# Kernel tuning notes

Hardware: AMD Instinct MI355X
Metric: run time of the kernel (lower is better)

Reference implementation:

```python
import jax, jax.numpy as jnp
from jax import lax
import numpy as np

N_VOX = 50000
B = 2
D, H, W = 8, 160, 160
CIN = 16
G = 3
K = 27
CHANS = [(16, 16), (16, 32), (32, 64), (64, 64), (64, 128)]
NAMES = ['in', 'e1', 'e2', 'e3', 'out']


def setup_inputs() -> dict:
    key = jax.random.key(0)
    ks = jax.random.split(key, 16)
    rng = np.random.default_rng(0)
    # unique active cells -> deterministic scatter/gather rulebook
    lin = rng.choice(B * D * H * W, size=N_VOX, replace=False)
    bz = lin // (D * H * W)
    rem = lin % (D * H * W)
    zz = rem // (H * W)
    yy = (rem % (H * W)) // W
    xx = rem % W
    coors = jnp.asarray(np.stack([bz, zz, yy, xx], 1).astype(np.int32))
    inp = {
        'voxel_features': jax.random.normal(ks[0], (N_VOX, CIN), jnp.float32),
        'coors': coors,
        'batch_size': B,
    }
    i = 1
    for nm, (ci, co) in zip(NAMES, CHANS):
        k1, k2 = jax.random.split(ks[i]); i += 1
        inp['wb_' + nm] = jax.random.normal(k1, (K, ci, co), jnp.float32) * 0.05
        inp['ws_' + nm] = jax.random.normal(k2, (K, ci, G, co), jnp.float32) * 0.05
        inp['gm_' + nm] = jnp.ones((co,), jnp.float32)
        inp['bt_' + nm] = jnp.zeros((co,), jnp.float32)
    return inp


def _kan_block(feat, nbr, wb, ws, gm, bt, centers, inv_h):
    # submanifold KAN conv: gather -> (silu base + RBF spline basis) GEMM -> accumulate
    n = feat.shape[0]
    fp = jnp.concatenate([feat, jnp.zeros((1, feat.shape[1]), feat.dtype)], 0)  # pad row for out-of-grid

    def body(acc, kin):
        idx, wbk, wsk = kin
        x = fp[idx]                                   # [N, Cin] gathered neighbors
        base = jax.nn.silu(x) @ wbk                   # [N, Cout]
        bas = jnp.exp(-jnp.square((x[:, :, None] - centers) * inv_h))  # [N, Cin, G]
        spl = jnp.einsum('ncg,cgo->no', bas, wsk)     # [N, Cout]
        return acc + base + spl, None

    out0 = jnp.zeros((n, wb.shape[-1]), feat.dtype)
    out, _ = lax.scan(jax.checkpoint(body), out0, (nbr, wb, ws))
    # BatchNorm1d (train-mode batch stats) + ReLU
    mu = out.mean(0)
    var = out.var(0)
    out = (out - mu) * lax.rsqrt(var + 1e-3) * gm + bt
    return jax.nn.relu(out)


def _build_rulebook(coors, batch_size, n):
    grid = jnp.full((batch_size, D + 2, H + 2, W + 2), n, jnp.int32)
    grid = grid.at[coors[:, 0], coors[:, 1] + 1, coors[:, 2] + 1, coors[:, 3] + 1].set(
        jnp.arange(n, dtype=jnp.int32))
    offs = [(dz, dy, dx) for dz in (-1, 0, 1) for dy in (-1, 0, 1) for dx in (-1, 0, 1)]
    return jnp.stack([
        grid[coors[:, 0], coors[:, 1] + 1 + dz, coors[:, 2] + 1 + dy, coors[:, 3] + 1 + dx]
        for dz, dy, dx in offs])  # [27, N]


def reference(voxel_features, coors, batch_size,
              wb_in, ws_in, gm_in, bt_in,
              wb_e1, ws_e1, gm_e1, bt_e1,
              wb_e2, ws_e2, gm_e2, bt_e2,
              wb_e3, ws_e3, gm_e3, bt_e3,
              wb_out, ws_out, gm_out, bt_out):
    n = voxel_features.shape[0]
    nbr = _build_rulebook(coors, batch_size, n)
    centers = jnp.linspace(-1.0, 1.0, G)
    inv_h = (G - 1) / 2.0
    x = _kan_block(voxel_features, nbr, wb_in, ws_in, gm_in, bt_in, centers, inv_h)
    x = _kan_block(x, nbr, wb_e1, ws_e1, gm_e1, bt_e1, centers, inv_h)
    x = _kan_block(x, nbr, wb_e2, ws_e2, gm_e2, bt_e2, centers, inv_h)
    x = _kan_block(x, nbr, wb_e3, ws_e3, gm_e3, bt_e3, centers, inv_h)
    x = _kan_block(x, nbr, wb_out, ws_out, gm_out, bt_out, centers, inv_h)
    co = x.shape[1]
    dense = jnp.zeros((batch_size, D, H, W, co), x.dtype)
    dense = dense.at[coors[:, 0], coors[:, 1], coors[:, 2], coors[:, 3]].set(x)
    dense = dense.transpose(0, 4, 1, 2, 3)            # [B, C, D, H, W]
    return dense.reshape(batch_size, co * D, H, W)    # [B, C*D, H, W]
```

## Files before the change

### kernel.cpp

```cpp
#include <hip/hip_runtime.h>

#define N_VOX 50000
#define BATCH 2
#define DD 8
#define HH 160
#define WW 160
#define PD 10
#define PH 162
#define PW 162
#define KK 27
#define NCELL (BATCH*DD*HH*WW)
#define GRID_ELEMS (BATCH*PD*PH*PW)
#define OUT_ELEMS (BATCH*128*DD*HH*WW)

typedef __attribute__((ext_vector_type(8))) short short8v;
typedef __attribute__((ext_vector_type(4))) float float4v;

__device__ inline unsigned short f2bf(float f) {
    unsigned u = __float_as_uint(f);
    u += 0x7FFFu + ((u >> 16) & 1u);
    return (unsigned short)(u >> 16);
}

__device__ inline void gload_lds16(const void* g, void* l) {
    __builtin_amdgcn_global_load_lds(
        (const __attribute__((address_space(1))) void*)g,
        (__attribute__((address_space(3))) void*)l, 16, 0, 0);
}

__global__ void k_flags(const int* __restrict__ coors, int* __restrict__ flags) {
    int n = blockIdx.x * 256 + threadIdx.x;
    if (n >= N_VOX) return;
    int b = coors[n*4+0], z = coors[n*4+1], y = coors[n*4+2], x = coors[n*4+3];
    flags[((b*DD + z)*HH + y)*WW + x] = 1;
}

__global__ void k_scan1(const int* __restrict__ flags, int* __restrict__ scanout,
                        int* __restrict__ bsums) {
    __shared__ int s[256];
    int t = threadIdx.x, blk = blockIdx.x;
    int4 v = ((const int4*)(flags + blk*1024))[t];
    int tsum = v.x + v.y + v.z + v.w;
    s[t] = tsum; __syncthreads();
    for (int off = 1; off < 256; off <<= 1) {
        int x = (t >= off) ? s[t-off] : 0;
        __syncthreads(); s[t] += x; __syncthreads();
    }
    int excl = s[t] - tsum;
    int4 o; o.x = excl; o.y = excl + v.x; o.z = o.y + v.y; o.w = o.z + v.z;
    ((int4*)(scanout + blk*1024))[t] = o;
    if (t == 255) bsums[blk] = s[255];
}

__global__ void k_scan2(int* __restrict__ bsums) {
    __shared__ int s[512];
    int t = threadIdx.x;
    int orig = (t < 400) ? bsums[t] : 0;
    s[t] = orig; __syncthreads();
    for (int off = 1; off < 512; off <<= 1) {
        int x = (t >= off) ? s[t-off] : 0;
        __syncthreads(); s[t] += x; __syncthreads();
    }
    if (t < 400) bsums[t] = s[t] - orig;
}

__global__ void k_pos(const float* __restrict__ vf, const int* __restrict__ coors,
                      const int* __restrict__ scanout, const int* __restrict__ bsums,
                      int* __restrict__ vox_at, int* __restrict__ gridP,
                      unsigned short* __restrict__ phi) {
    int n = blockIdx.x * 256 + threadIdx.x;
    if (n > N_VOX) return;
    if (n == N_VOX) {
        ushort4 p;
        p.x = f2bf(0.f);
        p.y = f2bf(__expf(-1.f));
        p.z = f2bf(1.f);
        p.w = f2bf(__expf(-1.f));
        #pragma unroll
        for (int c = 0; c < 16; ++c)
            *(ushort4*)&phi[((size_t)N_VOX * 16 + c) * 4] = p;
        return;
    }
    int b = coors[n*4+0], z = coors[n*4+1], y = coors[n*4+2], x = coors[n*4+3];
    int lin = ((b*DD + z)*HH + y)*WW + x;
    int pos = scanout[lin] + bsums[lin >> 10];
    vox_at[pos] = n;
    gridP[((b*PD + z+1)*PH + (y+1))*PW + (x+1)] = pos;
    #pragma unroll
    for (int c = 0; c < 16; ++c) {
        float xv = vf[(size_t)n * 16 + c];
        float sig = 1.f / (1.f + __expf(-xv));
        ushort4 p;
        p.x = f2bf(xv * sig);
        p.y = f2bf(__expf(-(xv + 1.f) * (xv + 1.f)));
        p.z = f2bf(__expf(-xv * xv));
        p.w = f2bf(__expf(-(xv - 1.f) * (xv - 1.f)));
        *(ushort4*)&phi[((size_t)pos * 16 + c) * 4] = p;
    }
}

__global__ void k_nbrP(const int* __restrict__ coors, const int* __restrict__ vox_at,
                       const int* __restrict__ gridP, int* __restrict__ nbrP) {
    int i = blockIdx.x * 256 + threadIdx.x;
    if (i >= N_VOX) return;
    int n = vox_at[i];
    int b = coors[n*4+0], z = coors[n*4+1]+1, y = coors[n*4+2]+1, x = coors[n*4+3]+1;
    int k = 0;
    for (int dz = -1; dz <= 1; ++dz)
        for (int dy = -1; dy <= 1; ++dy)
            for (int dx = -1; dx <= 1; ++dx) {
                int g = gridP[((b*PD + z+dz)*PH + (y+dy))*PW + (x+dx)];
                nbrP[k*N_VOX + i] = (g >= 0) ? g : N_VOX;
                ++k;
            }
}

struct WswzArgs {
    const float* wb[5];
    const float* ws[5];
    unsigned short* dst[5];
};
__global__ void k_wswz_all(WswzArgs a) {
    constexpr int off[6]   = {0, 27648, 82944, 304128, 746496, 1631232};
    constexpr int lgCI4[5] = {6, 6, 7, 8, 8};
    constexpr int lgCO[5]  = {4, 5, 6, 6, 7};
    int e = blockIdx.x * 256 + threadIdx.x;
    if (e >= off[5]) return;
    int L = 0;
    #pragma unroll
    for (int i = 1; i < 5; ++i) L += (e >= off[i]);
    int el = e - off[L];
    int CIN4 = 1 << lgCI4[L], COUT = 1 << lgCO[L], CIN = CIN4 >> 2;
    int j8   = el & 7;
    int rest = el >> 3;
    int o    = rest & (COUT - 1);
    int kb   = rest >> lgCO[L];
    int kabs = kb * 8 + j8;
    int k  = kabs >> lgCI4[L];
    int c4 = kabs & (CIN4 - 1);
    int c = c4 >> 2, jj = c4 & 3;
    float v = (jj == 0) ? a.wb[L][(k * CIN + c) * COUT + o]
                        : a.ws[L][((k * CIN + c) * 3 + (jj - 1)) * COUT + o];
    a.dst[L][el] = f2bf(v);
}

template<int CIN, int COUT, int NSPL>
__global__ __launch_bounds__(64, 2) void k_conv_mfma(
    const unsigned short* __restrict__ phi,
    const int*            __restrict__ nbrP,
    const unsigned short* __restrict__ Wsw,
    float*                __restrict__ pre,
    float*                __restrict__ sums)
{
    constexpr int CIN4   = CIN * 4;
    constexpr int BK     = 64;
    constexpr int SPK    = CIN4 / BK;
    constexpr int NSTAGE = KK * SPK;
    constexpr int COUTH  = COUT / NSPL;
    constexpr int NFW    = COUTH / 16;
    constexpr int WR     = 4;
    constexpr int NMB    = (N_VOX + 63) / 64;
    constexpr int NBLK   = NMB * NSPL;
    constexpr int PERX   = (NBLK + 7) / 8;

    int lb = blockIdx.x;
    int linear = (lb & 7) * PERX + (lb >> 3);
    if (linear >= NBLK) return;
    const int mb = linear / NSPL, h = linear % NSPL;

    const int lane = threadIdx.x & 63;
    const int l15 = lane & 15, q = lane >> 4;
    const int base = mb * 64;
    int vg[WR];
    #pragma unroll
    for (int rs = 0; rs < WR; ++rs) vg[rs] = base + rs * 16 + l15;
    const int ob = h * COUTH;

    const unsigned short* bp = Wsw + (size_t)(q * COUT + ob + l15) * 8;

    int rows[WR], rowsN[WR];
    short8v A0[2][WR], A1[2][WR];
    short8v B0[2][NFW], B1[2][NFW];

    auto loadB = [&](int sp, short8v (&Bb)[2][NFW]) {
        #pragma unroll
        for (int kk = 0; kk < 2; ++kk)
            #pragma unroll
            for (int nf = 0; nf < NFW; ++nf)
                Bb[kk][nf] = *(const short8v*)(bp +
                    ((size_t)(sp * 8 + kk * 4) * COUT + nf * 16) * 8);
    };
    auto loadA = [&](int sp, short8v (&Ab)[2][WR]) {
        if (sp % SPK == 0) {
            #pragma unroll
            for (int rs = 0; rs < WR; ++rs) rows[rs] = rowsN[rs];
        }
        const int c4s = (sp % SPK) * BK;
        #pragma unroll
        for (int rs = 0; rs < WR; ++rs) {
            const unsigned short* p = phi + (size_t)rows[rs] * CIN4 + c4s + q * 8;
            Ab[0][rs] = *(const short8v*)p;
            Ab[1][rs] = *(const short8v*)(p + 32);
        }
        if (sp % SPK == 0) {
            int k2 = sp / SPK + 1;
            if (k2 < KK) {
                #pragma unroll
                for (int rs = 0; rs < WR; ++rs)
                    rowsN[rs] = (vg[rs] < N_VOX) ? nbrP[k2 * N_VOX + vg[rs]] : N_VOX;
            }
        }
    };

    float4v acc[WR][NFW];
    #pragma unroll
    for (int rs = 0; rs < WR; ++rs)
        #pragma unroll
        for (int nf = 0; nf < NFW; ++nf)
            acc[rs][nf] = (float4v){0.f, 0.f, 0.f, 0.f};

    auto domfma = [&](const short8v (&Ab)[2][WR], const short8v (&Bb)[2][NFW]) {
        #pragma unroll
        for (int kk = 0; kk < 2; ++kk)
            #pragma unroll
            for (int nf = 0; nf < NFW; ++nf)
                #pragma unroll
                for (int rs = 0; rs < WR; ++rs)
                    acc[rs][nf] = __builtin_amdgcn_mfma_f32_16x16x32_bf16(
                        Ab[kk][rs], Bb[kk][nf], acc[rs][nf], 0, 0, 0);
    };

    #pragma unroll
    for (int rs = 0; rs < WR; ++rs) {
        rows[rs]  = (vg[rs] < N_VOX) ? nbrP[vg[rs]] : N_VOX;
        rowsN[rs] = (vg[rs] < N_VOX) ? nbrP[N_VOX + vg[rs]] : N_VOX;
    }
    loadB(0, B0);
    #pragma unroll
    for (int rs = 0; rs < WR; ++rs) {
        const unsigned short* p = phi + (size_t)rows[rs] * CIN4 + q * 8;
        A0[0][rs] = *(const short8v*)p;
        A0[1][rs] = *(const short8v*)(p + 32);
    }

    #define SLOT(T, Ac, Bc, An, Bn)                                   \
        if ((T) + 1 < NSTAGE) { loadB((T) + 1, Bn); loadA((T) + 1, An); } \
        __builtin_amdgcn_sched_barrier(0);                            \
        domfma(Ac, Bc);

    int s = 0;
    for (; s + 2 <= NSTAGE; s += 2) {
        SLOT(s + 0, A0, B0, A1, B1)
        SLOT(s + 1, A1, B1, A0, B0)
    }
    if constexpr (NSTAGE % 2 != 0) {
        domfma(A0, B0);
    }
    #undef SLOT

    #pragma unroll
    for (int rs = 0; rs < WR; ++rs)
        #pragma unroll
        for (int nf = 0; nf < NFW; ++nf)
            #pragma unroll
            for (int r = 0; r < 4; ++r) {
                int v = base + rs * 16 + q * 4 + r;
                if (v < N_VOX)
                    pre[(size_t)v * COUT + ob + nf * 16 + l15] = acc[rs][nf][r];
            }

    float* S = sums + (blockIdx.x & 7) * 256;
    #pragma unroll
    for (int nf = 0; nf < NFW; ++nf) {
        float s1 = 0.f, s2 = 0.f;
        #pragma unroll
        for (int rs = 0; rs < WR; ++rs)
            #pragma unroll
            for (int r = 0; r < 4; ++r) {
                int v = base + rs * 16 + q * 4 + r;
                if (v < N_VOX) {
                    float a = acc[rs][nf][r];
                    s1 += a; s2 += a * a;
                }
            }
        s1 += __shfl_xor(s1, 16); s1 += __shfl_xor(s1, 32);
        s2 += __shfl_xor(s2, 16); s2 += __shfl_xor(s2, 32);
        if (q == 0) {
            atomicAdd(&S[ob + nf * 16 + l15], s1);
            atomicAdd(&S[COUT + ob + nf * 16 + l15], s2);
        }
    }
}

template<int CIN, int COUT, int NSPL>
__global__ __launch_bounds__(512, 4) void k_conv_bsh(
    const unsigned short* __restrict__ phi,
    const int*            __restrict__ nbrP,
    const unsigned short* __restrict__ Wsw,
    float*                __restrict__ pre,
    float*                __restrict__ sums)
{
    constexpr int CIN4   = CIN * 4;
    constexpr int BK     = 64;
    constexpr int SPK    = CIN4 / BK;
    constexpr int NSTAGE = KK * SPK;
    constexpr int KB_G   = 8 * SPK;
    constexpr int COUTH  = COUT / NSPL;
    constexpr int NFW    = COUTH / 16;
    constexpr int WR     = 2;
    constexpr int NMB    = (N_VOX + 255) / 256;
    constexpr int NBLK   = NMB * NSPL;
    constexpr int PERX   = (NBLK + 7) / 8;
    constexpr int SI     = KB_G / 8;

    __shared__ short8v ldsB[2][KB_G][64];

    int lb = blockIdx.x;
    int linear = (lb & 7) * PERX + (lb >> 3);
    if (linear >= NBLK) return;
    const int mb = linear / NSPL, h = linear % NSPL;

    const int t = threadIdx.x, lane = t & 63, w = t >> 6;
    const int l15 = lane & 15, q = lane >> 4;
    const int base = mb * 256 + w * 32;
    int vg[WR];
    #pragma unroll
    for (int rs = 0; rs < WR; ++rs) vg[rs] = base + rs * 16 + l15;
    const int ob = h * COUTH;

    int rows[WR], rowsN[WR];
    short8v A0[2][WR], A1[2][WR];

    auto stage = [&](int g) {
        #pragma unroll
        for (int j = 0; j < SI; ++j) {
            const int m = w * SI + j;
            gload_lds16(Wsw + ((size_t)(g * KB_G + m) * COUT + ob + lane) * 8,
                        &ldsB[g & 1][m][0]);
        }
    };
    auto loadA = [&](int sp, short8v (&Ab)[2][WR]) {
        if (sp % SPK == 0) {
            #pragma unroll
            for (int rs = 0; rs < WR; ++rs) rows[rs] = rowsN[rs];
        }
        const int c4s = (sp % SPK) * BK;
        #pragma unroll
        for (int rs = 0; rs < WR; ++rs) {
            const unsigned short* p = phi + (size_t)rows[rs] * CIN4 + c4s + q * 8;
            Ab[0][rs] = *(const short8v*)p;
            Ab[1][rs] = *(const short8v*)(p + 32);
        }
        if (sp % SPK == 0) {
            int k2 = sp / SPK + 1;
            if (k2 < KK) {
                #pragma unroll
                for (int rs = 0; rs < WR; ++rs)
                    rowsN[rs] = (vg[rs] < N_VOX) ? nbrP[k2 * N_VOX + vg[rs]] : N_VOX;
            }
        }
    };

    float4v acc[WR][NFW];
    #pragma unroll
    for (int rs = 0; rs < WR; ++rs)
        #pragma unroll
        for (int nf = 0; nf < NFW; ++nf)
            acc[rs][nf] = (float4v){0.f, 0.f, 0.f, 0.f};

    stage(0);
    __builtin_amdgcn_sched_barrier(0);
    #pragma unroll
    for (int rs = 0; rs < WR; ++rs) {
        rows[rs]  = (vg[rs] < N_VOX) ? nbrP[vg[rs]] : N_VOX;
        rowsN[rs] = (vg[rs] < N_VOX) ? nbrP[N_VOX + vg[rs]] : N_VOX;
    }
    #pragma unroll
    for (int rs = 0; rs < WR; ++rs) {
        const unsigned short* p = phi + (size_t)rows[rs] * CIN4 + q * 8;
        A0[0][rs] = *(const short8v*)p;
        A0[1][rs] = *(const short8v*)(p + 32);
    }

    int sp = 0;
    #define SLOTB(SG, Ac, An)                                                 \
    {                                                                         \
        short8v bf[2][NFW];                                                   \
        _Pragma("unroll") for (int kk = 0; kk < 2; ++kk)                      \
        _Pragma("unroll") for (int nf = 0; nf < NFW; ++nf)                    \
            bf[kk][nf] = ldsB[g & 1][(SG) * 8 + kk * 4 + q][nf * 16 + l15];   \
        if (sp + 1 < NSTAGE) loadA(sp + 1, An);                               \
        __builtin_amdgcn_sched_barrier(0);                                    \
        _Pragma("unroll") for (int kk = 0; kk < 2; ++kk)                      \
        _Pragma("unroll") for (int nf = 0; nf < NFW; ++nf)                    \
        _Pragma("unroll") for (int rs = 0; rs < WR; ++rs)                     \
            acc[rs][nf] = __builtin_amdgcn_mfma_f32_16x16x32_bf16(            \
                Ac[kk][rs], bf[kk][nf], acc[rs][nf], 0, 0, 0);                \
        ++sp;                                                                 \
    }

    for (int g = 0; g < KK; ++g) {
        if (g == 0) {
            asm volatile("s_waitcnt vmcnt(8)" ::: "memory");
        } else if (g == KK - 1) {
            asm volatile("s_waitcnt vmcnt(%0)" :: "i"(4 * SPK) : "memory");
        } else {
            asm volatile("s_waitcnt vmcnt(%0)" :: "i"(4 * SPK + 2) : "memory");
        }
        __builtin_amdgcn_sched_barrier(0);
        __builtin_amdgcn_s_barrier();
        __builtin_amdgcn_sched_barrier(0);
        if (g + 1 < KK) stage(g + 1);
        __builtin_amdgcn_sched_barrier(0);
        SLOTB(0, A0, A1)
        SLOTB(1, A1, A0)
        if constexpr (SPK == 4) {
            SLOTB(2, A0, A1)
            SLOTB(3, A1, A0)
        }
    }
    #undef SLOTB

    #pragma unroll
    for (int rs = 0; rs < WR; ++rs)
        #pragma unroll
        for (int nf = 0; nf < NFW; ++nf)
            #pragma unroll
            for (int r = 0; r < 4; ++r) {
                int v = base + rs * 16 + q * 4 + r;
                if (v < N_VOX)
                    pre[(size_t)v * COUT + ob + nf * 16 + l15] = acc[rs][nf][r];
            }

    float* S = sums + (blockIdx.x & 7) * 256;
    #pragma unroll
    for (int nf = 0; nf < NFW; ++nf) {
        float s1 = 0.f, s2 = 0.f;
        #pragma unroll
        for (int rs = 0; rs < WR; ++rs)
            #pragma unroll
            for (int r = 0; r < 4; ++r) {
                int v = base + rs * 16 + q * 4 + r;
                if (v < N_VOX) {
                    float a = acc[rs][nf][r];
                    s1 += a; s2 += a * a;
                }
            }
        s1 += __shfl_xor(s1, 16); s1 += __shfl_xor(s1, 32);
        s2 += __shfl_xor(s2, 16); s2 += __shfl_xor(s2, 32);
        if (q == 0) {
            atomicAdd(&S[ob + nf * 16 + l15], s1);
            atomicAdd(&S[COUT + ob + nf * 16 + l15], s2);
        }
    }
}

template<int COUT>
__global__ void k_bnapply_phi(const float* __restrict__ pre, const float* __restrict__ sums,
                              const float* __restrict__ gm, const float* __restrict__ bt,
                              unsigned short* __restrict__ phi) {
    __shared__ float sc[COUT], sh[COUT];
    int t = threadIdx.x;
    if (t < COUT) {
        float s1 = 0.f, s2 = 0.f;
        #pragma unroll
        for (int xo = 0; xo < 8; ++xo) {
            s1 += sums[xo * 256 + t];
            s2 += sums[xo * 256 + COUT + t];
        }
        float mu  = s1 * (1.f / N_VOX);
        float var = s2 * (1.f / N_VOX) - mu*mu;
        float s = rsqrtf(var + 1e-3f) * gm[t];
        sc[t] = s;
        sh[t] = bt[t] - mu * s;
    }
    __syncthreads();
    int tot = (N_VOX + 1) * COUT;
    for (int e = blockIdx.x*256 + t; e < tot; e += gridDim.x*256) {
        int i = e / COUT, c = e % COUT;
        float x = 0.f;
        if (i < N_VOX) x = fmaxf(pre[(size_t)i*COUT + c] * sc[c] + sh[c], 0.f);
        float sig = 1.f / (1.f + __expf(-x));
        ushort4 p;
        p.x = f2bf(x * sig);
        p.y = f2bf(__expf(-(x + 1.f) * (x + 1.f)));
        p.z = f2bf(__expf(-x * x));
        p.w = f2bf(__expf(-(x - 1.f) * (x - 1.f)));
        *(ushort4*)&phi[(size_t)e * 4] = p;
    }
}

__global__ void k_bnfin(const float* __restrict__ sums, const float* __restrict__ gm,
                        const float* __restrict__ bt, float* __restrict__ scsh) {
    int t = threadIdx.x;
    float s1 = 0.f, s2 = 0.f;
    #pragma unroll
    for (int xo = 0; xo < 8; ++xo) {
        s1 += sums[xo * 256 + t];
        s2 += sums[xo * 256 + 128 + t];
    }
    float mu  = s1 * (1.f / N_VOX);
    float var = s2 * (1.f / N_VOX) - mu*mu;
    float s = rsqrtf(var + 1e-3f) * gm[t];
    scsh[t]       = s;
    scsh[128 + t] = bt[t] - mu * s;
}

__global__ void k_dense(const float* __restrict__ feat, const int* __restrict__ gridP,
                        const float* __restrict__ scsh, float* __restrict__ out) {
    int e4 = blockIdx.x*256 + threadIdx.x;
    if (e4 >= OUT_ELEMS/4) return;
    int e = e4 * 4;
    int x  = e % WW;
    int y  = (e / WW) % HH;
    int cz = (e / (WW*HH)) % (128*DD);
    int b  = e / (WW*HH*128*DD);
    int c = cz >> 3, z = cz & 7;
    float sc = scsh[c], sh = scsh[128 + c];
    const int* gp = &gridP[((b*PD + z+1)*PH + (y+1))*PW + (x+1)];
    int g0 = gp[0], g1 = gp[1], g2 = gp[2], g3 = gp[3];
    float4 o;
    o.x = (g0 >= 0) ? fmaxf(feat[(size_t)g0*128 + c] * sc + sh, 0.f) : 0.f;
    o.y = (g1 >= 0) ? fmaxf(feat[(size_t)g1*128 + c] * sc + sh, 0.f) : 0.f;
    o.z = (g2 >= 0) ? fmaxf(feat[(size_t)g2*128 + c] * sc + sh, 0.f) : 0.f;
    o.w = (g3 >= 0) ? fmaxf(feat[(size_t)g3*128 + c] * sc + sh, 0.f) : 0.f;
    *(float4*)&out[e] = o;
}

template<int CIN, int COUT, int NSPL>
static void run_block(const float* gm, const float* bt,
                      const int* nbrP, unsigned short* phi, const unsigned short* Wsw,
                      float* sums, float* pre, hipStream_t stream) {
    constexpr int NMB  = (N_VOX + 63) / 64;
    constexpr int NBLK = NMB * NSPL;
    constexpr int GRID = ((NBLK + 7) / 8) * 8;
    k_conv_mfma<CIN, COUT, NSPL><<<GRID, 64, 0, stream>>>(phi, nbrP, Wsw, pre, sums);
    k_bnapply_phi<COUT><<<512, 256, 0, stream>>>(pre, sums, gm, bt, phi);
}

template<int CIN, int COUT, int NSPL>
static void run_block_bsh(const float* gm, const float* bt,
                          const int* nbrP, unsigned short* phi, const unsigned short* Wsw,
                          float* sums, float* pre, bool last, hipStream_t stream) {
    constexpr int NMB  = (N_VOX + 255) / 256;
    constexpr int NBLK = NMB * NSPL;
    constexpr int GRID = ((NBLK + 7) / 8) * 8;
    k_conv_bsh<CIN, COUT, NSPL><<<GRID, 512, 0, stream>>>(phi, nbrP, Wsw, pre, sums);
    if (!last)
        k_bnapply_phi<COUT><<<512, 256, 0, stream>>>(pre, sums, gm, bt, phi);
}

extern "C" void kernel_launch(void* const* d_in, const int* in_sizes, int n_in,
                              void* d_out, int out_size, void* d_ws, size_t ws_size,
                              hipStream_t stream) {
    const float* vf    = (const float*)d_in[0];
    const int*   coors = (const int*)d_in[1];
    const float* wb[5] = {(const float*)d_in[3],  (const float*)d_in[7],
                          (const float*)d_in[11], (const float*)d_in[15],
                          (const float*)d_in[19]};
    const float* wsp[5]= {(const float*)d_in[4],  (const float*)d_in[8],
                          (const float*)d_in[12], (const float*)d_in[16],
                          (const float*)d_in[20]};
    const float* gm[5] = {(const float*)d_in[5],  (const float*)d_in[9],
                          (const float*)d_in[13], (const float*)d_in[17],
                          (const float*)d_in[21]};
    const float* bt[5] = {(const float*)d_in[6],  (const float*)d_in[10],
                          (const float*)d_in[14], (const float*)d_in[18],
                          (const float*)d_in[22]};

    char* p = (char*)d_ws;
    auto alloc = [&](size_t bytes) {
        char* r = p;
        p += (bytes + 255) & ~(size_t)255;
        return r;
    };
    int*            flags   = (int*)           alloc((size_t)NCELL * 4);
    int*            scanout = (int*)           alloc((size_t)NCELL * 4);
    int*            bsums   = (int*)           alloc(512 * 4);
    int*            vox_at  = (int*)           alloc((size_t)N_VOX * 4);
    int*            gridP   = (int*)           alloc((size_t)GRID_ELEMS * 4);
    int*            nbrP    = (int*)           alloc((size_t)KK * N_VOX * 4);
    unsigned short* Wsw0    = (unsigned short*)alloc((size_t)KK * 64  * 16  * 2);
    unsigned short* Wsw1    = (unsigned short*)alloc((size_t)KK * 64  * 32  * 2);
    unsigned short* Wsw2    = (unsigned short*)alloc((size_t)KK * 128 * 64  * 2);
    unsigned short* Wsw3    = (unsigned short*)alloc((size_t)KK * 256 * 64  * 2);
    unsigned short* Wsw4    = (unsigned short*)alloc((size_t)KK * 256 * 128 * 2);
    unsigned short* phi     = (unsigned short*)alloc((size_t)(N_VOX + 1) * 256 * 2);
    float*          sumsAll = (float*)         alloc(5 * 8 * 256 * 4);
    float*          pre     = (float*)         alloc((size_t)N_VOX * 128 * 4);
    float*          scsh    = (float*)         alloc(256 * 4);

    hipMemsetAsync(flags, 0, (size_t)NCELL * 4, stream);
    hipMemsetAsync(gridP, 0xFF, (size_t)GRID_ELEMS * 4, stream);
    hipMemsetAsync(sumsAll, 0, 5 * 8 * 256 * 4, stream);

    WswzArgs wa;
    for (int i = 0; i < 5; ++i) { wa.wb[i] = wb[i]; wa.ws[i] = wsp[i]; }
    wa.dst[0] = Wsw0; wa.dst[1] = Wsw1; wa.dst[2] = Wsw2; wa.dst[3] = Wsw3; wa.dst[4] = Wsw4;
    k_wswz_all<<<(1631232 + 255) / 256, 256, 0, stream>>>(wa);

    k_flags<<<(N_VOX+255)/256, 256, 0, stream>>>(coors, flags);
    k_scan1<<<NCELL/1024, 256, 0, stream>>>(flags, scanout, bsums);
    k_scan2<<<1, 512, 0, stream>>>(bsums);
    k_pos  <<<(N_VOX+1+255)/256, 256, 0, stream>>>(vf, coors, scanout, bsums,
                                                   vox_at, gridP, phi);
    k_nbrP <<<(N_VOX+255)/256, 256, 0, stream>>>(coors, vox_at, gridP, nbrP);

    run_block<16, 16, 1>(gm[0], bt[0], nbrP, phi, Wsw0, sumsAll + 0*2048, pre, stream);
    run_block<16, 32, 1>(gm[1], bt[1], nbrP, phi, Wsw1, sumsAll + 1*2048, pre, stream);
    run_block_bsh<32, 64,  1>(gm[2], bt[2], nbrP, phi, Wsw2, sumsAll + 2*2048, pre, false, stream);
    run_block_bsh<64, 64,  1>(gm[3], bt[3], nbrP, phi, Wsw3, sumsAll + 3*2048, pre, false, stream);
    run_block_bsh<64, 128, 2>(gm[4], bt[4], nbrP, phi, Wsw4, sumsAll + 4*2048, pre, true,  stream);

    k_bnfin<<<1, 128, 0, stream>>>(sumsAll + 4*2048, gm[4], bt[4], scsh);
    k_dense<<<(OUT_ELEMS/4 + 255)/256, 256, 0, stream>>>(pre, gridP, scsh, (float*)d_out);
}
```

Before: 614.7 us.

## Store intermediate pre-activations as bf16 and deepen A-operand prefetch to three buffers

For the intermediate blocks, the conv kernels now write pre-BN outputs as bf16 rather than fp32, and the BN-apply kernel reads them back as bf16. This halves that write and read traffic. The last block still writes fp32 for the dense scatter. The bsh conv kernel also gains a third A register buffer so gathered neighbour rows are prefetched two stages ahead, and each stage's B fragment loads are split into two halves; this costs more registers and adds bf16 rounding of the pre-BN values.

```diff
diff --git a/kernel.cpp b/kernel.cpp
--- a/kernel.cpp
+++ b/kernel.cpp
@@ -20,6 +20,9 @@
     unsigned u = __float_as_uint(f);
     u += 0x7FFFu + ((u >> 16) & 1u);
     return (unsigned short)(u >> 16);
+}
+__device__ inline float bf2f(unsigned short b) {
+    return __uint_as_float((unsigned)b << 16);
 }
 
 __device__ inline void gload_lds16(const void* g, void* l) {
@@ -149,7 +152,7 @@
     const unsigned short* __restrict__ phi,
     const int*            __restrict__ nbrP,
     const unsigned short* __restrict__ Wsw,
-    float*                __restrict__ pre,
+    unsigned short*       __restrict__ preB,
     float*                __restrict__ sums)
 {
     constexpr int CIN4   = CIN * 4;
@@ -266,7 +269,7 @@
             for (int r = 0; r < 4; ++r) {
                 int v = base + rs * 16 + q * 4 + r;
                 if (v < N_VOX)
-                    pre[(size_t)v * COUT + ob + nf * 16 + l15] = acc[rs][nf][r];
+                    preB[(size_t)v * COUT + ob + nf * 16 + l15] = f2bf(acc[rs][nf][r]);
             }
 
     float* S = sums + (blockIdx.x & 7) * 256;
@@ -292,12 +295,13 @@
     }
 }
 
-template<int CIN, int COUT, int NSPL>
+template<int CIN, int COUT, int NSPL, bool LAST>
 __global__ __launch_bounds__(512, 4) void k_conv_bsh(
     const unsigned short* __restrict__ phi,
     const int*            __restrict__ nbrP,
     const unsigned short* __restrict__ Wsw,
-    float*                __restrict__ pre,
+    float*                __restrict__ preF,
+    unsigned short*       __restrict__ preB,
     float*                __restrict__ sums)
 {
     constexpr int CIN4   = CIN * 4;
@@ -329,7 +333,7 @@
     const int ob = h * COUTH;
 
     int rows[WR], rowsN[WR];
-    short8v A0[2][WR], A1[2][WR];
+    short8v A0[2][WR], A1[2][WR], A2[2][WR];
 
     auto stage = [&](int g) {
         #pragma unroll
@@ -381,45 +385,58 @@
         A0[0][rs] = *(const short8v*)p;
         A0[1][rs] = *(const short8v*)(p + 32);
     }
-
-    int sp = 0;
-    #define SLOTB(SG, Ac, An)                                                 \
+    loadA(1, A1);
+
+    int sp = 0, g = 0;
+
+    #define SLOTX(Ac, An)                                                     \
     {                                                                         \
-        short8v bf[2][NFW];                                                   \
-        _Pragma("unroll") for (int kk = 0; kk < 2; ++kk)                      \
+        const int SG = sp % SPK; const int gb = g & 1;                        \
+        short8v bfv[NFW];                                                     \
         _Pragma("unroll") for (int nf = 0; nf < NFW; ++nf)                    \
-            bf[kk][nf] = ldsB[g & 1][(SG) * 8 + kk * 4 + q][nf * 16 + l15];   \
-        if (sp + 1 < NSTAGE) loadA(sp + 1, An);                               \
+            bfv[nf] = ldsB[gb][SG * 8 + q][nf * 16 + l15];                    \
+        if (sp + 2 < NSTAGE) loadA(sp + 2, An);                               \
         __builtin_amdgcn_sched_barrier(0);                                    \
-        _Pragma("unroll") for (int kk = 0; kk < 2; ++kk)                      \
         _Pragma("unroll") for (int nf = 0; nf < NFW; ++nf)                    \
         _Pragma("unroll") for (int rs = 0; rs < WR; ++rs)                     \
             acc[rs][nf] = __builtin_amdgcn_mfma_f32_16x16x32_bf16(            \
-                Ac[kk][rs], bf[kk][nf], acc[rs][nf], 0, 0, 0);                \
+                Ac[0][rs], bfv[nf], acc[rs][nf], 0, 0, 0);                    \
+        _Pragma("unroll") for (int nf = 0; nf < NFW; ++nf)                    \
+            bfv[nf] = ldsB[gb][SG * 8 + 4 + q][nf * 16 + l15];                \
+        _Pragma("unroll") for (int nf = 0; nf < NFW; ++nf)                    \
+        _Pragma("unroll") for (int rs = 0; rs < WR; ++rs)                     \
+            acc[rs][nf] = __builtin_amdgcn_mfma_f32_16x16x32_bf16(            \
+                Ac[1][rs], bfv[nf], acc[rs][nf], 0, 0, 0);                    \
         ++sp;                                                                 \
     }
 
-    for (int g = 0; g < KK; ++g) {
-        if (g == 0) {
-            asm volatile("s_waitcnt vmcnt(8)" ::: "memory");
-        } else if (g == KK - 1) {
-            asm volatile("s_waitcnt vmcnt(%0)" :: "i"(4 * SPK) : "memory");
+    #define GHDR                                                              \
+        if (g == 0) {                                                         \
+            asm volatile("s_waitcnt vmcnt(12)" ::: "memory");                 \
+        } else if (g == KK - 1) {                                             \
+            asm volatile("s_waitcnt vmcnt(%0)" :: "i"(4 * SPK) : "memory");   \
+        } else {                                                              \
+            asm volatile("s_waitcnt vmcnt(%0)" :: "i"(4 * SPK + 2) : "memory"); \
+        }                                                                     \
+        __builtin_amdgcn_sched_barrier(0);                                    \
+        __builtin_amdgcn_s_barrier();                                         \
+        __builtin_amdgcn_sched_barrier(0);                                    \
+        if (g + 1 < KK) stage(g + 1);                                         \
+        __builtin_amdgcn_sched_barrier(0);
+
+    for (int m = 0; m < KK / 3; ++m) {
+        if constexpr (SPK == 2) {
+            GHDR SLOTX(A0, A2) SLOTX(A1, A0) ++g;
+            GHDR SLOTX(A2, A1) SLOTX(A0, A2) ++g;
+            GHDR SLOTX(A1, A0) SLOTX(A2, A1) ++g;
         } else {
-            asm volatile("s_waitcnt vmcnt(%0)" :: "i"(4 * SPK + 2) : "memory");
-        }
-        __builtin_amdgcn_sched_barrier(0);
-        __builtin_amdgcn_s_barrier();
-        __builtin_amdgcn_sched_barrier(0);
-        if (g + 1 < KK) stage(g + 1);
-        __builtin_amdgcn_sched_barrier(0);
-        SLOTB(0, A0, A1)
-        SLOTB(1, A1, A0)
-        if constexpr (SPK == 4) {
-            SLOTB(2, A0, A1)
-            SLOTB(3, A1, A0)
-        }
-    }
-    #undef SLOTB
+            GHDR SLOTX(A0, A2) SLOTX(A1, A0) SLOTX(A2, A1) SLOTX(A0, A2) ++g;
+            GHDR SLOTX(A1, A0) SLOTX(A2, A1) SLOTX(A0, A2) SLOTX(A1, A0) ++g;
+            GHDR SLOTX(A2, A1) SLOTX(A0, A2) SLOTX(A1, A0) SLOTX(A2, A1) ++g;
+        }
+    }
+    #undef SLOTX
+    #undef GHDR
 
     #pragma unroll
     for (int rs = 0; rs < WR; ++rs)
@@ -428,8 +445,12 @@
             #pragma unroll
             for (int r = 0; r < 4; ++r) {
                 int v = base + rs * 16 + q * 4 + r;
-                if (v < N_VOX)
-                    pre[(size_t)v * COUT + ob + nf * 16 + l15] = acc[rs][nf][r];
+                if (v < N_VOX) {
+                    if constexpr (LAST)
+                        preF[(size_t)v * COUT + ob + nf * 16 + l15] = acc[rs][nf][r];
+                    else
+                        preB[(size_t)v * COUT + ob + nf * 16 + l15] = f2bf(acc[rs][nf][r]);
+                }
             }
 
     float* S = sums + (blockIdx.x & 7) * 256;
@@ -456,7 +477,8 @@
 }
 
 template<int COUT>
-__global__ void k_bnapply_phi(const float* __restrict__ pre, const float* __restrict__ sums,
+__global__ void k_bnapply_phi(const unsigned short* __restrict__ pre,
+                              const float* __restrict__ sums,
                               const float* __restrict__ gm, const float* __restrict__ bt,
                               unsigned short* __restrict__ phi) {
     __shared__ float sc[COUT], sh[COUT];
@@ -479,7 +501,8 @@
     for (int e = blockIdx.x*256 + t; e < tot; e += gridDim.x*256) {
         int i = e / COUT, c = e % COUT;
         float x = 0.f;
-        if (i < N_VOX) x = fmaxf(pre[(size_t)i*COUT + c] * sc[c] + sh[c], 0.f);
+        if (i < N_VOX)
+            x = fmaxf(bf2f(pre[(size_t)i*COUT + c]) * sc[c] + sh[c], 0.f);
         float sig = 1.f / (1.f + __expf(-x));
         ushort4 p;
         p.x = f2bf(x * sig);
@@ -530,24 +553,26 @@
 template<int CIN, int COUT, int NSPL>
 static void run_block(const float* gm, const float* bt,
                       const int* nbrP, unsigned short* phi, const unsigned short* Wsw,
-                      float* sums, float* pre, hipStream_t stream) {
+                      float* sums, unsigned short* preB, hipStream_t stream) {
     constexpr int NMB  = (N_VOX + 63) / 64;
     constexpr int NBLK = NMB * NSPL;
     constexpr int GRID = ((NBLK + 7) / 8) * 8;
-    k_conv_mfma<CIN, COUT, NSPL><<<GRID, 64, 0, stream>>>(phi, nbrP, Wsw, pre, sums);
-    k_bnapply_phi<COUT><<<512, 256, 0, stream>>>(pre, sums, gm, bt, phi);
-}
-
-template<int CIN, int COUT, int NSPL>
+    k_conv_mfma<CIN, COUT, NSPL><<<GRID, 64, 0, stream>>>(phi, nbrP, Wsw, preB, sums);
+    k_bnapply_phi<COUT><<<512, 256, 0, stream>>>(preB, sums, gm, bt, phi);
+}
+
+template<int CIN, int COUT, int NSPL, bool LAST>
 static void run_block_bsh(const float* gm, const float* bt,
                           const int* nbrP, unsigned short* phi, const unsigned short* Wsw,
-                          float* sums, float* pre, bool last, hipStream_t stream) {
+                          float* sums, float* preF, unsigned short* preB,
+                          hipStream_t stream) {
     constexpr int NMB  = (N_VOX + 255) / 256;
     constexpr int NBLK = NMB * NSPL;
     constexpr int GRID = ((NBLK + 7) / 8) * 8;
-    k_conv_bsh<CIN, COUT, NSPL><<<GRID, 512, 0, stream>>>(phi, nbrP, Wsw, pre, sums);
-    if (!last)
-        k_bnapply_phi<COUT><<<512, 256, 0, stream>>>(pre, sums, gm, bt, phi);
+    k_conv_bsh<CIN, COUT, NSPL, LAST><<<GRID, 512, 0, stream>>>(
+        phi, nbrP, Wsw, preF, preB, sums);
+    if constexpr (!LAST)
+        k_bnapply_phi<COUT><<<512, 256, 0, stream>>>(preB, sums, gm, bt, phi);
 }
 
 extern "C" void kernel_launch(void* const* d_in, const int* in_sizes, int n_in,
@@ -587,7 +612,8 @@
     unsigned short* Wsw4    = (unsigned short*)alloc((size_t)KK * 256 * 128 * 2);
     unsigned short* phi     = (unsigned short*)alloc((size_t)(N_VOX + 1) * 256 * 2);
     float*          sumsAll = (float*)         alloc(5 * 8 * 256 * 4);
-    float*          pre     = (float*)         alloc((size_t)N_VOX * 128 * 4);
+    float*          preF    = (float*)         alloc((size_t)N_VOX * 128 * 4);
+    unsigned short* preB    = (unsigned short*)alloc((size_t)N_VOX * 64 * 2);
     float*          scsh    = (float*)         alloc(256 * 4);
 
     hipMemsetAsync(flags, 0, (size_t)NCELL * 4, stream);
@@ -606,12 +632,12 @@
                                                    vox_at, gridP, phi);
     k_nbrP <<<(N_VOX+255)/256, 256, 0, stream>>>(coors, vox_at, gridP, nbrP);
 
-    run_block<16, 16, 1>(gm[0], bt[0], nbrP, phi, Wsw0, sumsAll + 0*2048, pre, stream);
-    run_block<16, 32, 1>(gm[1], bt[1], nbrP, phi, Wsw1, sumsAll + 1*2048, pre, stream);
-    run_block_bsh<32, 64,  1>(gm[2], bt[2], nbrP, phi, Wsw2, sumsAll + 2*2048, pre, false, stream);
-    run_block_bsh<64, 64,  1>(gm[3], bt[3], nbrP, phi, Wsw3, sumsAll + 3*2048, pre, false, stream);
-    run_block_bsh<64, 128, 2>(gm[4], bt[4], nbrP, phi, Wsw4, sumsAll + 4*2048, pre, true,  stream);
+    run_block<16, 16, 1>(gm[0], bt[0], nbrP, phi, Wsw0, sumsAll + 0*2048, preB, stream);
+    run_block<16, 32, 1>(gm[1], bt[1], nbrP, phi, Wsw1, sumsAll + 1*2048, preB, stream);
+    run_block_bsh<32, 64,  1, false>(gm[2], bt[2], nbrP, phi, Wsw2, sumsAll + 2*2048, preF, preB, stream);
+    run_block_bsh<64, 64,  1, false>(gm[3], bt[3], nbrP, phi, Wsw3, sumsAll + 3*2048, preF, preB, stream);
+    run_block_bsh<64, 128, 2, true >(gm[4], bt[4], nbrP, phi, Wsw4, sumsAll + 4*2048, preF, preB, stream);
 
     k_bnfin<<<1, 128, 0, stream>>>(sumsAll + 4*2048, gm[4], bt[4], scsh);
-    k_dense<<<(OUT_ELEMS/4 + 255)/256, 256, 0, stream>>>(pre, gridP, scsh, (float*)d_out);
-}
+    k_dense<<<(OUT_ELEMS/4 + 255)/256, 256, 0, stream>>>(preF, gridP, scsh, (float*)d_out);
+}
```

After: 631.2 us. 1.03x slower.
